# Performance work log

Hardware: AMD Instinct MI355X
Metric: run time of the kernel (lower is better)

The kernel has to match this reference:

```python
import jax, jax.numpy as jnp
import numpy as np

H = 256
NUM_CONVS = 4
NUM_GRAPHS = 1024
N_PER_GRAPH = 32
ORDER = 3
NUM_TYPES = 22  # len(utils.BOND_TYPES)
NUM_NOISE_LEVEL = 50
ANNEAL_POWER = 2.0


def _build_graph():
    # Chain molecules extended to order-3 neighbors (mimics extend_graph on a path graph):
    # for |i-j| in [1,ORDER]: edge_order=|i-j|, edge_type = bond type if order 1 else NUM_TYPES+order-1.
    n = N_PER_GRAPH
    i, j = np.meshgrid(np.arange(n), np.arange(n), indexing='ij')
    dist = np.abs(i - j)
    mask = (dist >= 1) & (dist <= ORDER)
    src_l, dst_l, eo = i[mask], j[mask], dist[mask]
    offs = np.arange(NUM_GRAPHS)[:, None] * n
    src = (src_l[None, :] + offs).reshape(-1)
    dst = (dst_l[None, :] + offs).reshape(-1)
    edge_order = np.tile(eo, NUM_GRAPHS)
    rng = np.random.default_rng(0)
    bond_t = rng.integers(1, 5, size=edge_order.shape)
    edge_type = np.where(edge_order == 1, bond_t, NUM_TYPES + edge_order - 1)
    node2graph = np.repeat(np.arange(NUM_GRAPHS), n)
    return src, dst, edge_type, node2graph


def setup_inputs() -> dict:
    key = jax.random.key(0)
    ks = jax.random.split(key, 24)
    src, dst, edge_type, node2graph = _build_graph()
    N, E = node2graph.shape[0], src.shape[0]
    w = lambda k, s: (jax.random.normal(k, s, jnp.float32) * 0.05)
    sigmas = jnp.asarray(np.exp(np.linspace(np.log(10.0), np.log(0.01), NUM_NOISE_LEVEL)), dtype=jnp.float32)
    return {
        'atom_type': jnp.asarray(np.random.default_rng(1).integers(0, 100, N), jnp.int32),
        'edge_index': jnp.asarray(np.stack([src, dst]), jnp.int32),
        'edge_type': jnp.asarray(edge_type, jnp.int32),
        'node2graph': jnp.asarray(node2graph, jnp.int32),
        'noise_level': jax.random.randint(ks[0], (NUM_GRAPHS,), 0, NUM_NOISE_LEVEL, jnp.int32),
        'pos': jax.random.normal(ks[1], (N, 3), jnp.float32) * 3.0,
        'd_noise': jax.random.normal(ks[2], (E, 1), jnp.float32),
        'sigmas': sigmas,
        'node_emb': w(ks[3], (100, H)), 'edge_emb': w(ks[4], (100, H)),
        'in_W1': w(ks[5], (1, H)), 'in_b1': w(ks[6], (H,)),
        'in_W2': w(ks[7], (H, H)), 'in_b2': w(ks[8], (H,)),
        'gin_W1': w(ks[9], (NUM_CONVS, H, H)), 'gin_b1': w(ks[10], (NUM_CONVS, H)),
        'gin_W2': w(ks[11], (NUM_CONVS, H, H)), 'gin_b2': w(ks[12], (NUM_CONVS, H)),
        'out_W1': w(ks[13], (2 * H, H)), 'out_b1': w(ks[14], (H,)),
        'out_W2': w(ks[15], (H, H // 2)), 'out_b2': w(ks[16], (H // 2,)),
        'out_W3': w(ks[17], (H // 2, 1)), 'out_b3': w(ks[18], (1,)),
    }


def reference(atom_type, edge_index, edge_type, node2graph, noise_level,
              pos, d_noise, sigmas, node_emb, edge_emb,
              in_W1, in_b1, in_W2, in_b2,
              gin_W1, gin_b1, gin_W2, gin_b2,
              out_W1, out_b1, out_W2, out_b2, out_W3, out_b3):
    N = pos.shape[0]
    G = noise_level.shape[0]
    row, col = edge_index[0], edge_index[1]
    edge2graph = node2graph[row]                                  # [E]
    d = jnp.linalg.norm(pos[row] - pos[col], axis=-1, keepdims=True)  # [E,1]
    used_sigmas = sigmas[noise_level][edge2graph][:, None]        # [E,1]
    perturbed_d = d + d_noise * used_sigmas
    target = -(perturbed_d - d) / used_sigmas ** 2
    # embeddings + input MLP (Linear-relu-Linear)
    node_attr = node_emb[atom_type]                               # [N,H]
    d_emb = jax.nn.relu(perturbed_d @ in_W1 + in_b1) @ in_W2 + in_b2
    edge_attr = d_emb * edge_emb[edge_type]                       # [E,H]
    # GIN with GINE convs: agg = sum_j relu(x_j + e_ij); out = MLP(x + agg); relu between convs; residual
    x = node_attr
    n_convs = gin_W1.shape[0]
    for k in range(n_convs):
        msg = jax.nn.relu(x[row] + edge_attr)                     # [E,H]
        agg = jax.ops.segment_sum(msg, col, num_segments=N)       # [N,H]
        h = jax.nn.relu((x + agg) @ gin_W1[k] + gin_b1[k]) @ gin_W2[k] + gin_b2[k]
        if k < n_convs - 1:
            h = jax.nn.relu(h)
        x = h + x  # short_cut
    # edge score head
    feat = jnp.concatenate([x[row] * x[col], edge_attr], axis=-1)  # [E,2H]
    s = jax.nn.relu(feat @ out_W1 + out_b1)
    s = jax.nn.relu(s @ out_W2 + out_b2)
    s = s @ out_W3 + out_b3                                       # [E,1]
    scores = (s / used_sigmas).reshape(-1)
    t = target.reshape(-1)
    loss_e = 0.5 * (scores - t) ** 2 * used_sigmas.reshape(-1) ** ANNEAL_POWER
    return jax.ops.segment_sum(loss_e, edge2graph, num_segments=G)  # [G]
```

## Files before the change

### kernel.cpp

```cpp
#include <hip/hip_runtime.h>
#include <math.h>

typedef unsigned int u32;
typedef __attribute__((ext_vector_type(2))) _Float16 h2;
typedef __attribute__((ext_vector_type(8))) _Float16 h8;
typedef __attribute__((ext_vector_type(4))) float f32x4;

#define MFMA16H(a,b,c) __builtin_amdgcn_mfma_f32_16x16x32_f16(a,b,c,0,0,0)

__device__ __forceinline__ u32 pkrtz(float a, float b){
  auto r = __builtin_amdgcn_cvt_pkrtz(a, b);
  return *(u32*)&r;
}
__device__ __forceinline__ uint4 pack8h(const float* f){
  uint4 v; v.x = pkrtz(f[0],f[1]); v.y = pkrtz(f[2],f[3]);
  v.z = pkrtz(f[4],f[5]); v.w = pkrtz(f[6],f[7]); return v;
}
__device__ __forceinline__ u32 pk_add(u32 a, u32 b){
  h2 r = *(h2*)&a + *(h2*)&b; return *(u32*)&r;
}
__device__ __forceinline__ u32 pk_mul(u32 a, u32 b){
  h2 r = *(h2*)&a * *(h2*)&b; return *(u32*)&r;
}
__device__ __forceinline__ u32 pk_relu(u32 a){
  h2 z = {(_Float16)0.f, (_Float16)0.f};
  h2 r = __builtin_elementwise_max(*(h2*)&a, z);
  return *(u32*)&r;
}

__device__ __forceinline__ void gload_lds16(const void* g, void* l){
  __builtin_amdgcn_global_load_lds((const __attribute__((address_space(1))) unsigned int*)g,
                                   (__attribute__((address_space(3))) unsigned int*)l,
                                   16, 0, 0);
}

__device__ __forceinline__ int frag_off(int f, int quad){
  return (f>>1)*64 + (f&1)*32 + ((quad ^ ((f>>1)&3))*8);
}

__device__ __forceinline__ int xg2(int g, int r){ return g ^ ((r ^ (g>>1)) & 7); }

__global__ void k_cvtAll(const float* __restrict__ inW2, const float* __restrict__ gW1,
                         const float* __restrict__ gW2, const float* __restrict__ oW1,
                         const float* __restrict__ oW2,
                         short* __restrict__ w2t, short* __restrict__ gw1t,
                         short* __restrict__ gw2t, short* __restrict__ ow1t,
                         short* __restrict__ ow2t){
  int gidx = blockIdx.x*256 + threadIdx.x;
  const float* src; short* dst; int t, K8, Nf;
  if (gidx < 8192)      { src = inW2; dst = w2t; t = gidx; K8 = 32; Nf = 256; }
  else if (gidx < 40960){ int r = gidx-8192;  int c = r>>13; t = r&8191;
                          src = gW1 + (size_t)c*65536; dst = gw1t + (size_t)c*65536; K8 = 32; Nf = 256; }
  else if (gidx < 73728){ int r = gidx-40960; int c = r>>13; t = r&8191;
                          src = gW2 + (size_t)c*65536; dst = gw2t + (size_t)c*65536; K8 = 32; Nf = 256; }
  else if (gidx < 90112){ t = gidx-73728; src = oW1; dst = ow1t; K8 = 64; Nf = 256; }
  else if (gidx < 94208){ t = gidx-90112; src = oW2; dst = ow2t; K8 = 32; Nf = 128; }
  else return;
  int f = t / K8, c = t - f*K8;
  float v[8];
  #pragma unroll
  for (int j=0;j<8;j++) v[j] = src[(size_t)(c*8+j)*Nf + f];
  ((uint4*)dst)[t] = pack8h(v);
}

__global__ void k_pre(const int* __restrict__ ei, const int* __restrict__ n2g,
                      const int* __restrict__ nl, const float* __restrict__ sigmas,
                      const float* __restrict__ pos, const float* __restrict__ dn, int E,
                      float* __restrict__ pd, int* __restrict__ cnt, int* __restrict__ inlist){
  int e = blockIdx.x*256 + threadIdx.x;
  if (e >= E) return;
  int r = ei[e], c = ei[E+e];
  float sg = sigmas[nl[n2g[r]]];
  float dx = pos[3*r]-pos[3*c], dy = pos[3*r+1]-pos[3*c+1], dz = pos[3*r+2]-pos[3*c+2];
  float d = sqrtf(dx*dx + dy*dy + dz*dz);
  pd[e] = d + dn[e]*sg;
  int slot = atomicAdd(&cnt[c], 1);
  if (slot < 8) inlist[c*8 + slot] = e;
}

__global__ __launch_bounds__(256) void k_attr(
    const float* __restrict__ pd, const float* __restrict__ W1, const float* __restrict__ b1,
    const short* __restrict__ W2t, const float* __restrict__ b2,
    const int* __restrict__ etype, const float* __restrict__ eemb,
    short* __restrict__ attr, int E)
{
  int tid = threadIdx.x;
  int base = blockIdx.x*64;
  int wv = tid>>6, lane = tid&63, quad = lane>>4, l15 = lane&15;
  float pdv[4];
  #pragma unroll
  for (int nt=0;nt<4;nt++) pdv[nt] = pd[base + nt*16 + l15];
  f32x4 acc[4][4];
  #pragma unroll
  for (int mt=0;mt<4;mt++) for (int nt=0;nt<4;nt++) acc[mt][nt] = (f32x4)0.f;
  #pragma unroll
  for (int s=0; s<8; s++){
    int k0 = s*32 + quad*8;
    float4 w1a = *(const float4*)(W1 + k0), w1b = *(const float4*)(W1 + k0 + 4);
    float4 b1a = *(const float4*)(b1 + k0), b1b = *(const float4*)(b1 + k0 + 4);
    h8 a[4], b[4];
    #pragma unroll
    for (int mt=0;mt<4;mt++){
      int f = (wv*4+mt)*16 + l15;
      a[mt] = *(const h8*)(W2t + (size_t)f*256 + k0);
    }
    #pragma unroll
    for (int nt=0;nt<4;nt++){
      float p = pdv[nt];
      float f[8] = {fmaxf(p*w1a.x+b1a.x,0.f), fmaxf(p*w1a.y+b1a.y,0.f),
                    fmaxf(p*w1a.z+b1a.z,0.f), fmaxf(p*w1a.w+b1a.w,0.f),
                    fmaxf(p*w1b.x+b1b.x,0.f), fmaxf(p*w1b.y+b1b.y,0.f),
                    fmaxf(p*w1b.z+b1b.z,0.f), fmaxf(p*w1b.w+b1b.w,0.f)};
      uint4 u = pack8h(f);
      b[nt] = *(h8*)&u;
    }
    #pragma unroll
    for (int mt=0;mt<4;mt++)
      #pragma unroll
      for (int nt=0;nt<4;nt++)
        acc[mt][nt] = MFMA16H(a[mt], b[nt], acc[mt][nt]);
  }
  #pragma unroll
  for (int nt=0;nt<4;nt++){
    int e = base + nt*16 + l15;
    int et = etype[e];
    #pragma unroll
    for (int mt=0;mt<4;mt++){
      int f0 = (wv*4+mt)*16 + quad*4;
      float4 bb = *(const float4*)(b2 + f0);
      float4 em = *(const float4*)(eemb + (size_t)et*256 + f0);
      float v0 = (acc[mt][nt][0]+bb.x)*em.x, v1 = (acc[mt][nt][1]+bb.y)*em.y;
      float v2 = (acc[mt][nt][2]+bb.z)*em.z, v3 = (acc[mt][nt][3]+bb.w)*em.w;
      uint2 v; v.x = pkrtz(v0,v1); v.y = pkrtz(v2,v3);
      *(uint2*)(attr + (size_t)e*256 + f0) = v;
    }
  }
}

__global__ __launch_bounds__(512,3) void k_conv4(
    const int* __restrict__ at, const float* __restrict__ nemb,
    const short* __restrict__ attrS, const int* __restrict__ ei,
    const int* __restrict__ cnt, const int* __restrict__ inlist,
    const short* __restrict__ gw1t, const float* __restrict__ gb1,
    const short* __restrict__ gw2t, const float* __restrict__ gb2,
    short* __restrict__ xF, int E)
{
  __shared__ short xls[33*256];
  __shared__ uint4 AlsV[32*32];
  __shared__ uint4 T1V [32*32];
  short* Als = (short*)AlsV;
  short* T1  = (short*)T1V;
  int tid = threadIdx.x;
  int nbase = blockIdx.x*32;
  int wv = tid>>6, lane = tid&63, quad = lane>>4, l15 = lane&15;
  int jl = tid>>4, ch = tid&15;

  int topo[8];
  {
    int j = nbase + jl;
    int deg = min(cnt[j], 8);
    int4 L0 = *(const int4*)(inlist + j*8);
    int4 L1 = *(const int4*)(inlist + j*8 + 4);
    int raw[8] = {L0.x,L0.y,L0.z,L0.w,L1.x,L1.y,L1.z,L1.w};
    #pragma unroll
    for (int s=0;s<8;s++){
      int e = (s < deg) ? raw[s] : E;
      int r = ei[e] - nbase;
      if (s >= deg) r = 32;
      topo[s] = e | (r << 20);
    }
  }
  {
    int a = at[nbase + jl];
    const float* src = nemb + (size_t)a*256 + ch*16;
    float f[16];
    #pragma unroll
    for (int q=0;q<4;q++){
      float4 v = *(const float4*)(src + q*4);
      f[q*4]=v.x; f[q*4+1]=v.y; f[q*4+2]=v.z; f[q*4+3]=v.w;
    }
    *(uint4*)(xls + jl*256 + xg2(ch*2,   jl)*8) = pack8h(f);
    *(uint4*)(xls + jl*256 + xg2(ch*2+1, jl)*8) = pack8h(f+8);
    if (tid < 32){ uint4 z; z.x=z.y=z.z=z.w=0u; ((uint4*)(xls + 32*256))[tid] = z; }
  }
  __syncthreads();
  for (int c=0; c<4; c++){
    const short* W1t = gw1t + (size_t)c*65536;
    const short* W2t = gw2t + (size_t)c*65536;
    const float* b1 = gb1 + c*256;
    const float* b2 = gb2 + c*256;
    {
      uint4 A0 = *(const uint4*)(xls + jl*256 + xg2(ch*2,   jl)*8);
      uint4 A1 = *(const uint4*)(xls + jl*256 + xg2(ch*2+1, jl)*8);
      #pragma unroll
      for (int s=0; s<8; s++){
        int e = topo[s] & 0xFFFFF;
        int r = topo[s] >> 20;
        uint4 x0 = *(const uint4*)(xls + r*256 + xg2(ch*2,   r)*8);
        uint4 x1 = *(const uint4*)(xls + r*256 + xg2(ch*2+1, r)*8);
        const short* ar = attrS + (size_t)e*256 + ch*16;
        uint4 a0 = *(const uint4*)(ar);
        uint4 a1 = *(const uint4*)(ar + 8);
        A0.x = pk_add(A0.x, pk_relu(pk_add(x0.x, a0.x)));
        A0.y = pk_add(A0.y, pk_relu(pk_add(x0.y, a0.y)));
        A0.z = pk_add(A0.z, pk_relu(pk_add(x0.z, a0.z)));
        A0.w = pk_add(A0.w, pk_relu(pk_add(x0.w, a0.w)));
        A1.x = pk_add(A1.x, pk_relu(pk_add(x1.x, a1.x)));
        A1.y = pk_add(A1.y, pk_relu(pk_add(x1.y, a1.y)));
        A1.z = pk_add(A1.z, pk_relu(pk_add(x1.z, a1.z)));
        A1.w = pk_add(A1.w, pk_relu(pk_add(x1.w, a1.w)));
      }
      *(uint4*)(Als + jl*256 + (((ch*2  ) ^ (jl&7))*8)) = A0;
      *(uint4*)(Als + jl*256 + (((ch*2+1) ^ (jl&7))*8)) = A1;
    }
    __syncthreads();
    f32x4 acc[2][2];
    #pragma unroll
    for (int mt=0;mt<2;mt++) for (int nt=0;nt<2;nt++) acc[mt][nt] = (f32x4)0.f;
    #pragma unroll
    for (int s=0; s<8; s++){
      h8 a[2], b[2];
      #pragma unroll
      for (int mt=0;mt<2;mt++)
        a[mt] = *(const h8*)(W1t + (size_t)((wv*2+mt)*16 + l15)*256 + s*32 + quad*8);
      #pragma unroll
      for (int nt=0;nt<2;nt++){
        int n = nt*16 + l15; int cc = s*4 + quad;
        b[nt] = *(const h8*)(Als + n*256 + ((cc ^ (n&7))*8));
      }
      #pragma unroll
      for (int mt=0;mt<2;mt++)
        #pragma unroll
        for (int nt=0;nt<2;nt++)
          acc[mt][nt] = MFMA16H(a[mt], b[nt], acc[mt][nt]);
    }
    #pragma unroll
    for (int mt=0;mt<2;mt++){
      int f0 = (wv*2+mt)*16 + quad*4;
      float4 bb = *(const float4*)(b1 + f0);
      int cg = f0 >> 3, off = (quad&1)*4;
      #pragma unroll
      for (int nt=0;nt<2;nt++){
        int n = nt*16 + l15;
        float v0 = fmaxf(acc[mt][nt][0]+bb.x,0.f), v1 = fmaxf(acc[mt][nt][1]+bb.y,0.f);
        float v2 = fmaxf(acc[mt][nt][2]+bb.z,0.f), v3 = fmaxf(acc[mt][nt][3]+bb.w,0.f);
        uint2 v; v.x = pkrtz(v0,v1); v.y = pkrtz(v2,v3);
        *(uint2*)(T1 + n*256 + ((cg ^ (n&7))*8) + off) = v;
      }
    }
    __syncthreads();
    f32x4 acc2[2][2];
    #pragma unroll
    for (int mt=0;mt<2;mt++) for (int nt=0;nt<2;nt++) acc2[mt][nt] = (f32x4)0.f;
    #pragma unroll
    for (int s=0; s<8; s++){
      h8 a[2], b[2];
      #pragma unroll
      for (int mt=0;mt<2;mt++)
        a[mt] = *(const h8*)(W2t + (size_t)((wv*2+mt)*16 + l15)*256 + s*32 + quad*8);
      #pragma unroll
      for (int nt=0;nt<2;nt++){
        int n = nt*16 + l15; int cc = s*4 + quad;
        b[nt] = *(const h8*)(T1 + n*256 + ((cc ^ (n&7))*8));
      }
      #pragma unroll
      for (int mt=0;mt<2;mt++)
        #pragma unroll
        for (int nt=0;nt<2;nt++)
          acc2[mt][nt] = MFMA16H(a[mt], b[nt], acc2[mt][nt]);
    }
    #pragma unroll
    for (int mt=0;mt<2;mt++){
      int f0 = (wv*2+mt)*16 + quad*4;
      float4 bb = *(const float4*)(b2 + f0);
      int g2 = f0 >> 3, half = (quad&1)*4;
      #pragma unroll
      for (int nt=0;nt<2;nt++){
        int n = nt*16 + l15;
        short* px = xls + n*256 + xg2(g2, n)*8 + half;
        uint2 old = *(uint2*)px;
        u32 n0 = pkrtz(acc2[mt][nt][0]+bb.x, acc2[mt][nt][1]+bb.y);
        u32 n1 = pkrtz(acc2[mt][nt][2]+bb.z, acc2[mt][nt][3]+bb.w);
        if (c < 3){ n0 = pk_relu(n0); n1 = pk_relu(n1); }
        uint2 v; v.x = pk_add(old.x, n0); v.y = pk_add(old.y, n1);
        *(uint2*)px = v;
      }
    }
    __syncthreads();
  }
  {
    uint4 v0 = *(const uint4*)(xls + jl*256 + xg2(ch*2,   jl)*8);
    uint4 v1 = *(const uint4*)(xls + jl*256 + xg2(ch*2+1, jl)*8);
    *(uint4*)(xF + (size_t)(nbase+jl)*256 + ch*16)     = v0;
    *(uint4*)(xF + (size_t)(nbase+jl)*256 + ch*16 + 8) = v1;
  }
}

__global__ __launch_bounds__(512,2) void k_head(
    const short* __restrict__ xF, const short* __restrict__ attrS,
    const int* __restrict__ ei,
    const short* __restrict__ W1t, const float* __restrict__ ob1,
    const short* __restrict__ W2t, const float* __restrict__ ob2,
    const float* __restrict__ W3, const float* __restrict__ ob3,
    const float* __restrict__ dnoise, const int* __restrict__ n2g,
    float* __restrict__ out, int E, int G)
{
  __shared__ uint4 BlsV[16*256];
  __shared__ float Sedge[64];
  __shared__ float part[4];
  short* Bls = (short*)BlsV;
  short* T   = (short*)BlsV;
  int tid = threadIdx.x;
  int base = blockIdx.x*64;
  int wv = tid>>6, lane = tid&63, quad = lane>>4, l15 = lane&15;
  if (tid < 64) Sedge[tid] = 0.f;
  if (tid < 4) part[tid] = 0.f;
  int g8 = tid & 255, sh = tid >> 8, w4 = g8 >> 6;
  {
    int p = g8>>3, hi = (g8>>2)&1, cs = g8&3;
    int n = p*2 + hi, cc = cs ^ (p&3);
    const short* srcb = attrS + (size_t)(base+n)*256 + cc*8;
    #pragma unroll
    for (int i=0;i<4;i++){
      int s = 8 + i*2 + sh;
      gload_lds16(srcb + (s-8)*32, (char*)BlsV + (size_t)s*4096 + w4*1024);
    }
  }
  {
    int p = g8>>3, hi = (g8>>2)&1, cs = g8&3;
    int n = p*2 + hi, cc = cs ^ (p&3);
    int rr = ei[base+n], rc = ei[E+base+n];
    const short* xr = xF + (size_t)rr*256 + cc*8;
    const short* xc = xF + (size_t)rc*256 + cc*8;
    #pragma unroll
    for (int i=0;i<4;i++){
      int s = sh*4 + i;
      uint4 va = *(const uint4*)(xr + s*32);
      uint4 vb = *(const uint4*)(xc + s*32);
      uint4 pr; pr.x = pk_mul(va.x, vb.x); pr.y = pk_mul(va.y, vb.y);
      pr.z = pk_mul(va.z, vb.z); pr.w = pk_mul(va.w, vb.w);
      *(uint4*)(Bls + (size_t)s*2048 + g8*8) = pr;
    }
  }
  __syncthreads();
  f32x4 acc[2][4];
  #pragma unroll
  for (int mt=0;mt<2;mt++) for (int nt=0;nt<4;nt++) acc[mt][nt] = (f32x4)0.f;
  #pragma unroll
  for (int s=0; s<16; s++){
    h8 a[2], b[4];
    #pragma unroll
    for (int mt=0;mt<2;mt++)
      a[mt] = *(const h8*)(W1t + (size_t)((wv*2+mt)*16 + l15)*512 + s*32 + quad*8);
    #pragma unroll
    for (int nt=0;nt<4;nt++)
      b[nt] = *(const h8*)(Bls + (size_t)s*2048 + frag_off(nt*16 + l15, quad));
    #pragma unroll
    for (int mt=0;mt<2;mt++)
      #pragma unroll
      for (int nt=0;nt<4;nt++)
        acc[mt][nt] = MFMA16H(a[mt], b[nt], acc[mt][nt]);
  }
  __syncthreads();
  #pragma unroll
  for (int mt=0;mt<2;mt++){
    int f0 = (wv*2+mt)*16 + quad*4;
    float4 bb = *(const float4*)(ob1 + f0);
    int c = f0 >> 3, off = (quad&1)*4;
    #pragma unroll
    for (int nt=0;nt<4;nt++){
      int n = nt*16 + l15;
      float v0 = fmaxf(acc[mt][nt][0]+bb.x,0.f), v1 = fmaxf(acc[mt][nt][1]+bb.y,0.f);
      float v2 = fmaxf(acc[mt][nt][2]+bb.z,0.f), v3 = fmaxf(acc[mt][nt][3]+bb.w,0.f);
      uint2 v; v.x = pkrtz(v0,v1); v.y = pkrtz(v2,v3);
      *(uint2*)(T + n*256 + ((c ^ (n&7))*8) + off) = v;
    }
  }
  __syncthreads();
  f32x4 acc2[4];
  #pragma unroll
  for (int nt=0;nt<4;nt++) acc2[nt] = (f32x4)0.f;
  #pragma unroll
  for (int s=0; s<8; s++){
    h8 a = *(const h8*)(W2t + (size_t)(wv*16 + l15)*256 + s*32 + quad*8);
    #pragma unroll
    for (int nt=0;nt<4;nt++){
      int n = nt*16 + l15; int cc = s*4 + quad;
      h8 b = *(const h8*)(T + n*256 + ((cc ^ (n&7))*8));
      acc2[nt] = MFMA16H(a, b, acc2[nt]);
    }
  }
  {
    int f0 = wv*16 + quad*4;
    float4 bb = *(const float4*)(ob2 + f0);
    float4 w3 = *(const float4*)(W3 + f0);
    #pragma unroll
    for (int nt=0;nt<4;nt++){
      float p = fmaxf(acc2[nt][0]+bb.x,0.f)*w3.x + fmaxf(acc2[nt][1]+bb.y,0.f)*w3.y
              + fmaxf(acc2[nt][2]+bb.z,0.f)*w3.z + fmaxf(acc2[nt][3]+bb.w,0.f)*w3.w;
      p += __shfl_xor(p, 16);
      p += __shfl_xor(p, 32);
      if (lane < 16) atomicAdd(&Sedge[nt*16 + l15], p);
    }
  }
  __syncthreads();
  int gbase = n2g[ei[base]];
  if (tid < 64){
    int e = base + tid;
    float sv = Sedge[tid] + ob3[0] + dnoise[e];
    float l = 0.5f*sv*sv;
    int g = n2g[ei[e]] - gbase;
    atomicAdd(&part[g & 3], l);
  }
  __syncthreads();
  if (tid < 2 && (gbase + tid) < G)
    atomicAdd(&out[gbase + tid], part[tid]);
}

static inline size_t alignup(size_t v){ return (v + 255) & ~(size_t)255; }

extern "C" void kernel_launch(void* const* d_in, const int* in_sizes, int n_in,
                              void* d_out, int out_size, void* d_ws, size_t ws_size,
                              hipStream_t stream) {
  const int*   at    = (const int*)  d_in[0];
  const int*   ei    = (const int*)  d_in[1];
  const int*   etype = (const int*)  d_in[2];
  const int*   n2g   = (const int*)  d_in[3];
  const int*   nl    = (const int*)  d_in[4];
  const float* pos   = (const float*)d_in[5];
  const float* dnoi  = (const float*)d_in[6];
  const float* sig   = (const float*)d_in[7];
  const float* nemb  = (const float*)d_in[8];
  const float* eemb  = (const float*)d_in[9];
  const float* inW1  = (const float*)d_in[10];
  const float* inb1  = (const float*)d_in[11];
  const float* inW2  = (const float*)d_in[12];
  const float* inb2  = (const float*)d_in[13];
  const float* gW1   = (const float*)d_in[14];
  const float* gb1   = (const float*)d_in[15];
  const float* gW2   = (const float*)d_in[16];
  const float* gb2   = (const float*)d_in[17];
  const float* oW1   = (const float*)d_in[18];
  const float* ob1   = (const float*)d_in[19];
  const float* oW2   = (const float*)d_in[20];
  const float* ob2   = (const float*)d_in[21];
  const float* oW3   = (const float*)d_in[22];
  const float* ob3   = (const float*)d_in[23];
  float* out = (float*)d_out;

  const int N = in_sizes[0];
  const int E = in_sizes[2];
  const int G = in_sizes[4];
  const int H = 256;

  char* w = (char*)d_ws;
  size_t off = 0;
  size_t o_attr  = off; off = alignup(off + (size_t)(E+1)*H*2);
  size_t o_xF    = off; off = alignup(off + (size_t)N*H*2);
  size_t o_pd    = off; off = alignup(off + (size_t)E*4);
  size_t o_cnt   = off; off = alignup(off + (size_t)N*4);
  size_t o_inl   = off; off = alignup(off + (size_t)N*8*4);
  size_t o_w2t   = off; off = alignup(off + (size_t)H*H*2);
  size_t o_gw1t  = off; off = alignup(off + (size_t)4*H*H*2);
  size_t o_gw2t  = off; off = alignup(off + (size_t)4*H*H*2);
  size_t o_ow1t  = off; off = alignup(off + (size_t)H*2*H*2);
  size_t o_ow2t  = off; off = alignup(off + (size_t)(H/2)*H*2);
  (void)ws_size; (void)n_in; (void)out_size;

  short* attrS = (short*)(w + o_attr);
  short* xF    = (short*)(w + o_xF);
  float* pd    = (float*)(w + o_pd);
  int*   cnt   = (int*)  (w + o_cnt);
  int*   inl   = (int*)  (w + o_inl);
  short* w2t   = (short*)(w + o_w2t);
  short* gw1t  = (short*)(w + o_gw1t);
  short* gw2t  = (short*)(w + o_gw2t);
  short* ow1t  = (short*)(w + o_ow1t);
  short* ow2t  = (short*)(w + o_ow2t);

  hipMemsetAsync(cnt, 0, (size_t)N*4, stream);
  hipMemsetAsync(out, 0, (size_t)G*4, stream);
  hipMemsetAsync(attrS + (size_t)E*H, 0, (size_t)H*2, stream);

  k_cvtAll<<<368, 256, 0, stream>>>(inW2, gW1, gW2, oW1, oW2,
                                    w2t, gw1t, gw2t, ow1t, ow2t);

  k_pre<<<(E+255)/256, 256, 0, stream>>>(ei, n2g, nl, sig, pos, dnoi, E, pd, cnt, inl);
  k_attr<<<E/64, 256, 0, stream>>>(pd, inW1, inb1, w2t, inb2, etype, eemb, attrS, E);

  k_conv4<<<G, 512, 0, stream>>>(at, nemb, attrS, ei, cnt, inl,
                                 gw1t, gb1, gw2t, gb2, xF, E);

  k_head<<<E/64, 512, 0, stream>>>(xF, attrS, ei, ow1t, ob1, ow2t, ob2,
                                   oW3, ob3, dnoi, n2g, out, E, G);
}
```

Measured before the change: 540.4 us.

## Process two graphs per conv block to double weight reuse per MFMA tile

The fused GIN conv kernel now handles 64 nodes (two graphs) per block instead of 32. Each wave computes 4 N-tiles, so every weight fragment loaded from global memory feeds twice as many MFMAs, and half as many blocks each stream the full weight set. LDS is reduced by aliasing the T1 buffer onto the aggregation buffer, which needs an extra barrier. Bounds checks cover an odd node count. Costs are more accumulator registers per thread, while the launch bound asks for higher occupancy.

```diff
diff --git a/kernel.cpp b/kernel.cpp
--- a/kernel.cpp
+++ b/kernel.cpp
@@ -137,51 +137,53 @@
   }
 }
 
-__global__ __launch_bounds__(512,3) void k_conv4(
+__global__ __launch_bounds__(512,4) void k_conv4(
     const int* __restrict__ at, const float* __restrict__ nemb,
     const short* __restrict__ attrS, const int* __restrict__ ei,
     const int* __restrict__ cnt, const int* __restrict__ inlist,
     const short* __restrict__ gw1t, const float* __restrict__ gb1,
     const short* __restrict__ gw2t, const float* __restrict__ gb2,
-    short* __restrict__ xF, int E)
+    short* __restrict__ xF, int E, int N)
 {
-  __shared__ short xls[33*256];
-  __shared__ uint4 AlsV[32*32];
-  __shared__ uint4 T1V [32*32];
+  __shared__ short xls[65*256];
+  __shared__ uint4 AlsV[64*32];
   short* Als = (short*)AlsV;
-  short* T1  = (short*)T1V;
+  short* T1  = (short*)AlsV;
   int tid = threadIdx.x;
-  int nbase = blockIdx.x*32;
+  int nbase = blockIdx.x*64;
   int wv = tid>>6, lane = tid&63, quad = lane>>4, l15 = lane&15;
-  int jl = tid>>4, ch = tid&15;
+  int jl = tid>>3, ch4 = tid&7;
 
   int topo[8];
   {
     int j = nbase + jl;
-    int deg = min(cnt[j], 8);
-    int4 L0 = *(const int4*)(inlist + j*8);
-    int4 L1 = *(const int4*)(inlist + j*8 + 4);
+    int jj = (j < N) ? j : 0;
+    int deg = (j < N) ? min(cnt[jj], 8) : 0;
+    int4 L0 = *(const int4*)(inlist + jj*8);
+    int4 L1 = *(const int4*)(inlist + jj*8 + 4);
     int raw[8] = {L0.x,L0.y,L0.z,L0.w,L1.x,L1.y,L1.z,L1.w};
     #pragma unroll
     for (int s=0;s<8;s++){
       int e = (s < deg) ? raw[s] : E;
       int r = ei[e] - nbase;
-      if (s >= deg) r = 32;
+      if (s >= deg) r = 64;
       topo[s] = e | (r << 20);
     }
   }
   {
-    int a = at[nbase + jl];
-    const float* src = nemb + (size_t)a*256 + ch*16;
-    float f[16];
+    int j = nbase + jl;
+    int a = (j < N) ? at[j] : 0;
+    const float* src = nemb + (size_t)a*256 + ch4*32;
     #pragma unroll
     for (int q=0;q<4;q++){
-      float4 v = *(const float4*)(src + q*4);
-      f[q*4]=v.x; f[q*4+1]=v.y; f[q*4+2]=v.z; f[q*4+3]=v.w;
-    }
-    *(uint4*)(xls + jl*256 + xg2(ch*2,   jl)*8) = pack8h(f);
-    *(uint4*)(xls + jl*256 + xg2(ch*2+1, jl)*8) = pack8h(f+8);
-    if (tid < 32){ uint4 z; z.x=z.y=z.z=z.w=0u; ((uint4*)(xls + 32*256))[tid] = z; }
+      float f[8];
+      float4 v0 = *(const float4*)(src + q*8);
+      float4 v1 = *(const float4*)(src + q*8 + 4);
+      f[0]=v0.x; f[1]=v0.y; f[2]=v0.z; f[3]=v0.w;
+      f[4]=v1.x; f[5]=v1.y; f[6]=v1.z; f[7]=v1.w;
+      *(uint4*)(xls + jl*256 + xg2(ch4*4+q, jl)*8) = pack8h(f);
+    }
+    if (tid < 32){ uint4 z; z.x=z.y=z.z=z.w=0u; ((uint4*)(xls + 64*256))[tid] = z; }
   }
   __syncthreads();
   for (int c=0; c<4; c++){
@@ -190,17 +192,23 @@
     const float* b1 = gb1 + c*256;
     const float* b2 = gb2 + c*256;
     {
-      uint4 A0 = *(const uint4*)(xls + jl*256 + xg2(ch*2,   jl)*8);
-      uint4 A1 = *(const uint4*)(xls + jl*256 + xg2(ch*2+1, jl)*8);
+      uint4 A0 = *(const uint4*)(xls + jl*256 + xg2(ch4*4,   jl)*8);
+      uint4 A1 = *(const uint4*)(xls + jl*256 + xg2(ch4*4+1, jl)*8);
+      uint4 A2 = *(const uint4*)(xls + jl*256 + xg2(ch4*4+2, jl)*8);
+      uint4 A3 = *(const uint4*)(xls + jl*256 + xg2(ch4*4+3, jl)*8);
       #pragma unroll
       for (int s=0; s<8; s++){
         int e = topo[s] & 0xFFFFF;
         int r = topo[s] >> 20;
-        uint4 x0 = *(const uint4*)(xls + r*256 + xg2(ch*2,   r)*8);
-        uint4 x1 = *(const uint4*)(xls + r*256 + xg2(ch*2+1, r)*8);
-        const short* ar = attrS + (size_t)e*256 + ch*16;
+        const short* ar = attrS + (size_t)e*256 + ch4*32;
+        uint4 x0 = *(const uint4*)(xls + r*256 + xg2(ch4*4,   r)*8);
+        uint4 x1 = *(const uint4*)(xls + r*256 + xg2(ch4*4+1, r)*8);
+        uint4 x2 = *(const uint4*)(xls + r*256 + xg2(ch4*4+2, r)*8);
+        uint4 x3 = *(const uint4*)(xls + r*256 + xg2(ch4*4+3, r)*8);
         uint4 a0 = *(const uint4*)(ar);
         uint4 a1 = *(const uint4*)(ar + 8);
+        uint4 a2 = *(const uint4*)(ar + 16);
+        uint4 a3 = *(const uint4*)(ar + 24);
         A0.x = pk_add(A0.x, pk_relu(pk_add(x0.x, a0.x)));
         A0.y = pk_add(A0.y, pk_relu(pk_add(x0.y, a0.y)));
         A0.z = pk_add(A0.z, pk_relu(pk_add(x0.z, a0.z)));
@@ -209,38 +217,49 @@
         A1.y = pk_add(A1.y, pk_relu(pk_add(x1.y, a1.y)));
         A1.z = pk_add(A1.z, pk_relu(pk_add(x1.z, a1.z)));
         A1.w = pk_add(A1.w, pk_relu(pk_add(x1.w, a1.w)));
+        A2.x = pk_add(A2.x, pk_relu(pk_add(x2.x, a2.x)));
+        A2.y = pk_add(A2.y, pk_relu(pk_add(x2.y, a2.y)));
+        A2.z = pk_add(A2.z, pk_relu(pk_add(x2.z, a2.z)));
+        A2.w = pk_add(A2.w, pk_relu(pk_add(x2.w, a2.w)));
+        A3.x = pk_add(A3.x, pk_relu(pk_add(x3.x, a3.x)));
+        A3.y = pk_add(A3.y, pk_relu(pk_add(x3.y, a3.y)));
+        A3.z = pk_add(A3.z, pk_relu(pk_add(x3.z, a3.z)));
+        A3.w = pk_add(A3.w, pk_relu(pk_add(x3.w, a3.w)));
       }
-      *(uint4*)(Als + jl*256 + (((ch*2  ) ^ (jl&7))*8)) = A0;
-      *(uint4*)(Als + jl*256 + (((ch*2+1) ^ (jl&7))*8)) = A1;
+      *(uint4*)(Als + jl*256 + (((ch4*4  ) ^ (jl&7))*8)) = A0;
+      *(uint4*)(Als + jl*256 + (((ch4*4+1) ^ (jl&7))*8)) = A1;
+      *(uint4*)(Als + jl*256 + (((ch4*4+2) ^ (jl&7))*8)) = A2;
+      *(uint4*)(Als + jl*256 + (((ch4*4+3) ^ (jl&7))*8)) = A3;
     }
     __syncthreads();
-    f32x4 acc[2][2];
-    #pragma unroll
-    for (int mt=0;mt<2;mt++) for (int nt=0;nt<2;nt++) acc[mt][nt] = (f32x4)0.f;
+    f32x4 acc[2][4];
+    #pragma unroll
+    for (int mt=0;mt<2;mt++) for (int nt=0;nt<4;nt++) acc[mt][nt] = (f32x4)0.f;
     #pragma unroll
     for (int s=0; s<8; s++){
-      h8 a[2], b[2];
+      h8 a[2], b[4];
       #pragma unroll
       for (int mt=0;mt<2;mt++)
         a[mt] = *(const h8*)(W1t + (size_t)((wv*2+mt)*16 + l15)*256 + s*32 + quad*8);
       #pragma unroll
-      for (int nt=0;nt<2;nt++){
+      for (int nt=0;nt<4;nt++){
         int n = nt*16 + l15; int cc = s*4 + quad;
         b[nt] = *(const h8*)(Als + n*256 + ((cc ^ (n&7))*8));
       }
       #pragma unroll
       for (int mt=0;mt<2;mt++)
         #pragma unroll
-        for (int nt=0;nt<2;nt++)
+        for (int nt=0;nt<4;nt++)
           acc[mt][nt] = MFMA16H(a[mt], b[nt], acc[mt][nt]);
     }
+    __syncthreads();
     #pragma unroll
     for (int mt=0;mt<2;mt++){
       int f0 = (wv*2+mt)*16 + quad*4;
       float4 bb = *(const float4*)(b1 + f0);
       int cg = f0 >> 3, off = (quad&1)*4;
       #pragma unroll
-      for (int nt=0;nt<2;nt++){
+      for (int nt=0;nt<4;nt++){
         int n = nt*16 + l15;
         float v0 = fmaxf(acc[mt][nt][0]+bb.x,0.f), v1 = fmaxf(acc[mt][nt][1]+bb.y,0.f);
         float v2 = fmaxf(acc[mt][nt][2]+bb.z,0.f), v3 = fmaxf(acc[mt][nt][3]+bb.w,0.f);
@@ -249,24 +268,24 @@
       }
     }
     __syncthreads();
-    f32x4 acc2[2][2];
-    #pragma unroll
-    for (int mt=0;mt<2;mt++) for (int nt=0;nt<2;nt++) acc2[mt][nt] = (f32x4)0.f;
+    f32x4 acc2[2][4];
+    #pragma unroll
+    for (int mt=0;mt<2;mt++) for (int nt=0;nt<4;nt++) acc2[mt][nt] = (f32x4)0.f;
     #pragma unroll
     for (int s=0; s<8; s++){
-      h8 a[2], b[2];
+      h8 a[2], b[4];
       #pragma unroll
       for (int mt=0;mt<2;mt++)
         a[mt] = *(const h8*)(W2t + (size_t)((wv*2+mt)*16 + l15)*256 + s*32 + quad*8);
       #pragma unroll
-      for (int nt=0;nt<2;nt++){
+      for (int nt=0;nt<4;nt++){
         int n = nt*16 + l15; int cc = s*4 + quad;
         b[nt] = *(const h8*)(T1 + n*256 + ((cc ^ (n&7))*8));
       }
       #pragma unroll
       for (int mt=0;mt<2;mt++)
         #pragma unroll
-        for (int nt=0;nt<2;nt++)
+        for (int nt=0;nt<4;nt++)
           acc2[mt][nt] = MFMA16H(a[mt], b[nt], acc2[mt][nt]);
     }
     #pragma unroll
@@ -275,7 +294,7 @@
       float4 bb = *(const float4*)(b2 + f0);
       int g2 = f0 >> 3, half = (quad&1)*4;
       #pragma unroll
-      for (int nt=0;nt<2;nt++){
+      for (int nt=0;nt<4;nt++){
         int n = nt*16 + l15;
         short* px = xls + n*256 + xg2(g2, n)*8 + half;
         uint2 old = *(uint2*)px;
@@ -288,11 +307,12 @@
     }
     __syncthreads();
   }
-  {
-    uint4 v0 = *(const uint4*)(xls + jl*256 + xg2(ch*2,   jl)*8);
-    uint4 v1 = *(const uint4*)(xls + jl*256 + xg2(ch*2+1, jl)*8);
-    *(uint4*)(xF + (size_t)(nbase+jl)*256 + ch*16)     = v0;
-    *(uint4*)(xF + (size_t)(nbase+jl)*256 + ch*16 + 8) = v1;
+  if (nbase + jl < N){
+    #pragma unroll
+    for (int q=0;q<4;q++){
+      uint4 v = *(const uint4*)(xls + jl*256 + xg2(ch4*4+q, jl)*8);
+      *(uint4*)(xF + (size_t)(nbase+jl)*256 + ch4*32 + q*8) = v;
+    }
   }
 }
 
@@ -488,8 +508,8 @@
   k_pre<<<(E+255)/256, 256, 0, stream>>>(ei, n2g, nl, sig, pos, dnoi, E, pd, cnt, inl);
   k_attr<<<E/64, 256, 0, stream>>>(pd, inW1, inb1, w2t, inb2, etype, eemb, attrS, E);
 
-  k_conv4<<<G, 512, 0, stream>>>(at, nemb, attrS, ei, cnt, inl,
-                                 gw1t, gb1, gw2t, gb2, xF, E);
+  k_conv4<<<(G+1)/2, 512, 0, stream>>>(at, nemb, attrS, ei, cnt, inl,
+                                       gw1t, gb1, gw2t, gb2, xF, E, N);
 
   k_head<<<E/64, 512, 0, stream>>>(xF, attrS, ei, ow1t, ob1, ow2t, ob2,
                                    oW3, ob3, dnoi, n2g, out, E, G);
```

Result: slower. 569.8 us (+5.4%).
